# Kernel tuning notes

Measured on AMD Instinct MI355X. Metric: run time of the kernel, lower is better.

## Reference

```python
import jax, jax.numpy as jnp
import numpy as np

B, S, H, I, E, K = 2, 512, 512, 1024, 64, 4


def setup_inputs() -> dict:
    key = jax.random.key(0)
    ks = jax.random.split(key, 16)
    scale = jnp.float32(0.02)

    def w(k, shape):
        return jax.random.normal(k, shape, dtype=jnp.float32) * scale

    return {
        "x": jax.random.normal(ks[0], (B, S, H), dtype=jnp.float32),
        "router_w": w(ks[1], (E, H)),
        "router_b": w(ks[2], (E,)),
        "expert_biases": jnp.zeros((E,), dtype=jnp.float32),
        "sw1": w(ks[3], (I, H)), "sb1": w(ks[4], (I,)),
        "sw2": w(ks[5], (H, I)), "sb2": w(ks[6], (H,)),
        "sw3": w(ks[7], (I, H)), "sb3": w(ks[8], (I,)),
        "w1": w(ks[9], (E, I, H)), "b1": w(ks[10], (E, I)),
        "w2": w(ks[11], (E, H, I)), "b2": w(ks[12], (E, H)),
        "w3": w(ks[13], (E, I, H)), "b3": w(ks[14], (E, I)),
        "top_k": K,
    }


def _ffn(x, w1, b1, w2, b2, w3, b3):
    return (jax.nn.silu(x @ w1.T + b1) * (x @ w3.T + b3)) @ w2.T + b2


def reference(x, router_w, router_b, expert_biases,
              sw1, sb1, sw2, sb2, sw3, sb3,
              w1, b1, w2, b2, w3, b3, top_k):
    Bx, Sx, Hx = x.shape
    Ex = router_w.shape[0]

    # Router: logits [B,S,E]; top-k selection uses bias-adjusted logits,
    # but gates come from the ORIGINAL (unbiased) logits.
    logits = x @ router_w.T + router_b
    _, idx = jax.lax.top_k(logits + expert_biases, top_k)  # [B,S,K] int32
    orig = jnp.take_along_axis(logits, idx, axis=-1)       # [B,S,K]
    scores = jax.nn.sigmoid(orig)
    gates = scores / jnp.maximum(jnp.sum(scores, axis=-1, keepdims=True), 1e-12)

    # Shared expert(s): num_shared_experts == 1, divided by 1.
    shared = _ffn(x, sw1, sb1, sw2, sb2, sw3, sb3)

    # Combine gates into a dense per-token per-expert gate matrix [T,E].
    xf = x.reshape(-1, Hx)                 # [T,H]
    T = xf.shape[0]
    tok = jnp.arange(T)[:, None]
    gate_full = jnp.zeros((T, Ex), x.dtype).at[tok, idx.reshape(T, top_k)].add(
        gates.reshape(T, top_k))

    # Routed experts: each expert FFN over all tokens, gated combine.
    # (Mathematically identical to the original masked-dense loop: the mask
    #  zeroes both inputs and gates of unassigned tokens.)
    def body(acc, p):
        ew1, eb1, ew2, eb2, ew3, eb3, g = p
        y = _ffn(xf, ew1, eb1, ew2, eb2, ew3, eb3)  # [T,H]
        return acc + g[:, None] * y, None

    acc, _ = jax.lax.scan(body, jnp.zeros_like(xf),
                          (w1, b1, w2, b2, w3, b3, gate_full.T))

    return shared + acc.reshape(x.shape)
```

## Files before the change

kernel.cpp:

```cpp
#include <hip/hip_runtime.h>
#include <math.h>

#define T_    1024
#define H_    512
#define I_    1024
#define E_    64
#define K_    4
#define NPAIR (T_*K_)
#define NENT  (NPAIR + T_)

#define BM 64
#define BN 64
#define BKS 64
#define LDP 72
#define MAXWORK 160

typedef float  f32x4  __attribute__((ext_vector_type(4)));
typedef short  bf16x8 __attribute__((ext_vector_type(8)));

__device__ __forceinline__ ushort f2bf(float f) {
    uint u = __float_as_uint(f);
    u += 0x7fffu + ((u >> 16) & 1u);
    return (ushort)(u >> 16);
}

__global__ __launch_bounds__(64) void moe_router(
    const float* __restrict__ x, const float* __restrict__ rw,
    const float* __restrict__ rb, const float* __restrict__ eb,
    int* __restrict__ idx_out, float* __restrict__ gate_out)
{
    const int t = blockIdx.x;
    const int lane = threadIdx.x;
    __shared__ float xs[H_];
    __shared__ float lg[E_];
    __shared__ float bs[E_];
    for (int i = lane; i < H_; i += 64) xs[i] = x[(size_t)t*H_ + i];
    bs[lane] = eb[lane];
    __syncthreads();
    float acc = 0.f;
    const float* wrow = rw + (size_t)lane*H_;
    for (int k = 0; k < H_; k += 4) {
        float4 w4 = *reinterpret_cast<const float4*>(wrow + k);
        acc = fmaf(xs[k+0], w4.x, acc);
        acc = fmaf(xs[k+1], w4.y, acc);
        acc = fmaf(xs[k+2], w4.z, acc);
        acc = fmaf(xs[k+3], w4.w, acc);
    }
    lg[lane] = acc + rb[lane];
    __syncthreads();
    if (lane == 0) {
        unsigned long long used = 0ull;
        int sel[K_]; float orig[K_];
        for (int k = 0; k < K_; ++k) {
            float best = -INFINITY; int bi = 0;
            for (int e = 0; e < E_; ++e) {
                if (used & (1ull << e)) continue;
                float v = lg[e] + bs[e];
                if (v > best) { best = v; bi = e; }
            }
            used |= (1ull << bi);
            sel[k] = bi; orig[k] = lg[bi];
        }
        float s[K_]; float sum = 0.f;
        for (int k = 0; k < K_; ++k) { s[k] = 1.f/(1.f + __expf(-orig[k])); sum += s[k]; }
        sum = fmaxf(sum, 1e-12f);
        for (int k = 0; k < K_; ++k) {
            idx_out[t*K_ + k] = sel[k];
            gate_out[t*K_ + k] = s[k] / sum;
        }
    }
}

__global__ __launch_bounds__(256) void moe_build(
    const int* __restrict__ idx, const float* __restrict__ gates,
    int* __restrict__ cnts, int* __restrict__ offs,
    int* __restrict__ entry_token, float* __restrict__ entry_gate,
    int* __restrict__ pair_pos,
    int* __restrict__ blk_e, int* __restrict__ blk_ro, int* __restrict__ nwork)
{
    __shared__ int c[E_];
    __shared__ int run[E_];
    const int tid = threadIdx.x;
    if (tid < E_) c[tid] = 0;
    __syncthreads();
    for (int p = tid; p < NPAIR; p += 256) atomicAdd(&c[idx[p]], 1);
    __syncthreads();
    if (tid == 0) {
        int o = 0;
        for (int e = 0; e < E_; ++e) { run[e] = o; offs[e] = o; cnts[e] = c[e]; o += c[e]; }
        offs[E_] = NPAIR;
        cnts[E_] = T_;
        int nb = 0;
        for (int e = 0; e <= E_; ++e) {
            int n = (e < E_) ? c[e] : T_;
            for (int ro = 0; ro < n; ro += BM) { blk_e[nb] = e; blk_ro[nb] = ro; ++nb; }
        }
        nwork[0] = nb;
    }
    __syncthreads();
    for (int p = tid; p < NPAIR; p += 256) {
        int e = idx[p];
        int pos = atomicAdd(&run[e], 1);
        entry_token[pos] = p / K_;
        entry_gate[pos]  = gates[p];
        pair_pos[p]      = pos;
    }
    for (int t = tid; t < T_; t += 256) {
        entry_token[NPAIR + t] = t;
        entry_gate[NPAIR + t]  = 1.0f;
    }
}

__global__ __launch_bounds__(256) void moe_stage1(
    const float* __restrict__ x,
    const float* __restrict__ w1, const float* __restrict__ b1,
    const float* __restrict__ w3, const float* __restrict__ b3,
    const float* __restrict__ sw1, const float* __restrict__ sb1,
    const float* __restrict__ sw3, const float* __restrict__ sb3,
    const int* __restrict__ cnts, const int* __restrict__ offs,
    const int* __restrict__ entry_token,
    const int* __restrict__ blk_e, const int* __restrict__ blk_ro,
    const int* __restrict__ nwork,
    ushort* __restrict__ h1buf)
{
    const int w = blockIdx.x;
    if (w >= nwork[0]) return;
    const int e  = blk_e[w];
    const int ro = blk_ro[w];
    const int itile = blockIdx.y;
    const int n = cnts[e];
    const int off = offs[e];
    const int rows = min(BM, n - ro);
    const float* W1 = (e < E_) ? (w1 + (size_t)e*I_*H_) : sw1;
    const float* W3 = (e < E_) ? (w3 + (size_t)e*I_*H_) : sw3;
    const float* B1 = (e < E_) ? (b1 + (size_t)e*I_) : sb1;
    const float* B3 = (e < E_) ? (b3 + (size_t)e*I_) : sb3;

    __shared__ ushort Xs [BM][LDP];
    __shared__ ushort W1s[BN][LDP];
    __shared__ ushort W3s[BN][LDP];

    const int tid  = threadIdx.x;
    const int lane = tid & 63;
    const int wid  = tid >> 6;
    const int wm   = wid >> 1;
    const int wn   = wid & 1;
    const int l15  = lane & 15;
    const int lg   = lane >> 4;

    f32x4 acc1[2][2] = {};
    f32x4 acc3[2][2] = {};

    for (int kc = 0; kc < H_; kc += BKS) {
        __syncthreads();
        #pragma unroll
        for (int i = 0; i < 4; ++i) {
            int u = tid + i*256;
            int r = u >> 4, seg = u & 15;
            float4 v = make_float4(0.f,0.f,0.f,0.f);
            if (r < rows) {
                int tok = entry_token[off + ro + r];
                v = *reinterpret_cast<const float4*>(x + (size_t)tok*H_ + kc + seg*4);
            }
            *reinterpret_cast<ushort4*>(&Xs[r][seg*4]) =
                make_ushort4(f2bf(v.x), f2bf(v.y), f2bf(v.z), f2bf(v.w));
        }
        #pragma unroll
        for (int i = 0; i < 4; ++i) {
            int u = tid + i*256;
            int r = u >> 4, seg = u & 15;
            size_t go = (size_t)(itile*BN + r)*H_ + kc + seg*4;
            float4 v1 = *reinterpret_cast<const float4*>(W1 + go);
            float4 v3 = *reinterpret_cast<const float4*>(W3 + go);
            *reinterpret_cast<ushort4*>(&W1s[r][seg*4]) =
                make_ushort4(f2bf(v1.x), f2bf(v1.y), f2bf(v1.z), f2bf(v1.w));
            *reinterpret_cast<ushort4*>(&W3s[r][seg*4]) =
                make_ushort4(f2bf(v3.x), f2bf(v3.y), f2bf(v3.z), f2bf(v3.w));
        }
        __syncthreads();
        #pragma unroll
        for (int s = 0; s < 2; ++s) {
            bf16x8 a[2], bb1[2], bb3[2];
            #pragma unroll
            for (int f = 0; f < 2; ++f) {
                a[f]   = *reinterpret_cast<const bf16x8*>(&Xs [wm*32 + f*16 + l15][s*32 + lg*8]);
                bb1[f] = *reinterpret_cast<const bf16x8*>(&W1s[wn*32 + f*16 + l15][s*32 + lg*8]);
                bb3[f] = *reinterpret_cast<const bf16x8*>(&W3s[wn*32 + f*16 + l15][s*32 + lg*8]);
            }
            #pragma unroll
            for (int fm = 0; fm < 2; ++fm) {
                #pragma unroll
                for (int fn = 0; fn < 2; ++fn) {
                    acc1[fm][fn] = __builtin_amdgcn_mfma_f32_16x16x32_bf16(a[fm], bb1[fn], acc1[fm][fn], 0, 0, 0);
                    acc3[fm][fn] = __builtin_amdgcn_mfma_f32_16x16x32_bf16(a[fm], bb3[fn], acc3[fm][fn], 0, 0, 0);
                }
            }
        }
    }
    #pragma unroll
    for (int fm = 0; fm < 2; ++fm) {
        #pragma unroll
        for (int fn = 0; fn < 2; ++fn) {
            const int col = itile*BN + wn*32 + fn*16 + l15;
            const float bv1 = B1[col];
            const float bv3 = B3[col];
            #pragma unroll
            for (int j = 0; j < 4; ++j) {
                const int rl = wm*32 + fm*16 + lg*4 + j;
                if (rl < rows) {
                    float z1 = acc1[fm][fn][j] + bv1;
                    float z3 = acc3[fm][fn][j] + bv3;
                    float h = z1 / (1.f + __expf(-z1)) * z3;
                    h1buf[(size_t)(off+ro+rl)*I_ + col] = f2bf(h);
                }
            }
        }
    }
}

__global__ __launch_bounds__(256) void moe_stage2(
    const ushort* __restrict__ h1buf,
    const float* __restrict__ w2, const float* __restrict__ b2,
    const float* __restrict__ sw2, const float* __restrict__ sb2,
    const int* __restrict__ cnts, const int* __restrict__ offs,
    const float* __restrict__ entry_gate,
    const int* __restrict__ blk_e, const int* __restrict__ blk_ro,
    const int* __restrict__ nwork,
    float* __restrict__ ybuf)
{
    const int w = blockIdx.x;
    if (w >= nwork[0]) return;
    const int e  = blk_e[w];
    const int ro = blk_ro[w];
    const int htile = blockIdx.y;
    const int n = cnts[e];
    const int off = offs[e];
    const int rows = min(BM, n - ro);
    const float* W2 = (e < E_) ? (w2 + (size_t)e*H_*I_) : sw2;
    const float* B2 = (e < E_) ? (b2 + (size_t)e*H_) : sb2;

    __shared__ ushort Hs[BM][LDP];
    __shared__ ushort Ws[BN][LDP];

    const int tid  = threadIdx.x;
    const int lane = tid & 63;
    const int wid  = tid >> 6;
    const int wm   = wid >> 1;
    const int wn   = wid & 1;
    const int l15  = lane & 15;
    const int lg   = lane >> 4;

    f32x4 acc[2][2] = {};

    for (int kc = 0; kc < I_; kc += BKS) {
        __syncthreads();
        #pragma unroll
        for (int i = 0; i < 2; ++i) {
            int u = tid + i*256;
            int r = u >> 3, seg = u & 7;
            uint4 v = make_uint4(0u,0u,0u,0u);
            if (r < rows)
                v = *reinterpret_cast<const uint4*>(h1buf + (size_t)(off+ro+r)*I_ + kc + seg*8);
            *reinterpret_cast<uint4*>(&Hs[r][seg*8]) = v;
        }
        #pragma unroll
        for (int i = 0; i < 4; ++i) {
            int u = tid + i*256;
            int r = u >> 4, seg = u & 15;
            size_t go = (size_t)(htile*BN + r)*I_ + kc + seg*4;
            float4 v = *reinterpret_cast<const float4*>(W2 + go);
            *reinterpret_cast<ushort4*>(&Ws[r][seg*4]) =
                make_ushort4(f2bf(v.x), f2bf(v.y), f2bf(v.z), f2bf(v.w));
        }
        __syncthreads();
        #pragma unroll
        for (int s = 0; s < 2; ++s) {
            bf16x8 a[2], b[2];
            #pragma unroll
            for (int f = 0; f < 2; ++f) {
                a[f] = *reinterpret_cast<const bf16x8*>(&Hs[wm*32 + f*16 + l15][s*32 + lg*8]);
                b[f] = *reinterpret_cast<const bf16x8*>(&Ws[wn*32 + f*16 + l15][s*32 + lg*8]);
            }
            #pragma unroll
            for (int fm = 0; fm < 2; ++fm) {
                #pragma unroll
                for (int fn = 0; fn < 2; ++fn) {
                    acc[fm][fn] = __builtin_amdgcn_mfma_f32_16x16x32_bf16(a[fm], b[fn], acc[fm][fn], 0, 0, 0);
                }
            }
        }
    }
    #pragma unroll
    for (int fm = 0; fm < 2; ++fm) {
        #pragma unroll
        for (int fn = 0; fn < 2; ++fn) {
            const int col = htile*BN + wn*32 + fn*16 + l15;
            const float bv = B2[col];
            #pragma unroll
            for (int j = 0; j < 4; ++j) {
                const int rl = wm*32 + fm*16 + lg*4 + j;
                if (rl < rows) {
                    const float g = entry_gate[off + ro + rl];
                    ybuf[(size_t)(off+ro+rl)*H_ + col] = (acc[fm][fn][j] + bv) * g;
                }
            }
        }
    }
}

__global__ __launch_bounds__(128) void moe_combine(
    const float* __restrict__ ybuf, const int* __restrict__ pair_pos,
    float* __restrict__ out)
{
    const int t = blockIdx.x;
    const int lane = threadIdx.x;
    const int h = lane * 4;
    const int p0 = pair_pos[t*K_+0], p1 = pair_pos[t*K_+1];
    const int p2 = pair_pos[t*K_+2], p3 = pair_pos[t*K_+3];
    float4 a  = *reinterpret_cast<const float4*>(ybuf + (size_t)(NPAIR+t)*H_ + h);
    float4 v0 = *reinterpret_cast<const float4*>(ybuf + (size_t)p0*H_ + h);
    float4 v1 = *reinterpret_cast<const float4*>(ybuf + (size_t)p1*H_ + h);
    float4 v2 = *reinterpret_cast<const float4*>(ybuf + (size_t)p2*H_ + h);
    float4 v3 = *reinterpret_cast<const float4*>(ybuf + (size_t)p3*H_ + h);
    float4 r;
    r.x = a.x + v0.x + v1.x + v2.x + v3.x;
    r.y = a.y + v0.y + v1.y + v2.y + v3.y;
    r.z = a.z + v0.z + v1.z + v2.z + v3.z;
    r.w = a.w + v0.w + v1.w + v2.w + v3.w;
    *reinterpret_cast<float4*>(out + (size_t)t*H_ + h) = r;
}

extern "C" void kernel_launch(void* const* d_in, const int* in_sizes, int n_in,
                              void* d_out, int out_size, void* d_ws, size_t ws_size,
                              hipStream_t stream)
{
    const float* x   = (const float*)d_in[0];
    const float* rw  = (const float*)d_in[1];
    const float* rb  = (const float*)d_in[2];
    const float* eb  = (const float*)d_in[3];
    const float* sw1 = (const float*)d_in[4];
    const float* sb1 = (const float*)d_in[5];
    const float* sw2 = (const float*)d_in[6];
    const float* sb2 = (const float*)d_in[7];
    const float* sw3 = (const float*)d_in[8];
    const float* sb3 = (const float*)d_in[9];
    const float* w1  = (const float*)d_in[10];
    const float* b1  = (const float*)d_in[11];
    const float* w2  = (const float*)d_in[12];
    const float* b2  = (const float*)d_in[13];
    const float* w3  = (const float*)d_in[14];
    const float* b3  = (const float*)d_in[15];
    float* out = (float*)d_out;

    char* p = (char*)d_ws;
    auto take = [&](size_t bytes) { char* q = p; p += (bytes + 255) & ~(size_t)255; return q; };
    int*    idxb  = (int*)   take((size_t)NPAIR*4);
    float*  gateb = (float*) take((size_t)NPAIR*4);
    int*    cnts  = (int*)   take((E_+1)*4);
    int*    offs  = (int*)   take((E_+1)*4);
    int*    etok  = (int*)   take((size_t)NENT*4);
    float*  egate = (float*) take((size_t)NENT*4);
    int*    ppos  = (int*)   take((size_t)NPAIR*4);
    int*    blk_e = (int*)   take((size_t)MAXWORK*4);
    int*    blk_ro= (int*)   take((size_t)MAXWORK*4);
    int*    nwork = (int*)   take(4);
    ushort* h1buf = (ushort*)take((size_t)NENT*I_*2);
    float*  ybuf  = (float*) take((size_t)NENT*H_*4);

    moe_router <<<T_, 64, 0, stream>>>(x, rw, rb, eb, idxb, gateb);
    moe_build  <<<1, 256, 0, stream>>>(idxb, gateb, cnts, offs, etok, egate, ppos,
                                       blk_e, blk_ro, nwork);
    moe_stage1 <<<dim3(MAXWORK, I_/BN), 256, 0, stream>>>(x, w1, b1, w3, b3,
                                                          sw1, sb1, sw3, sb3,
                                                          cnts, offs, etok,
                                                          blk_e, blk_ro, nwork, h1buf);
    moe_stage2 <<<dim3(MAXWORK, H_/BN), 256, 0, stream>>>(h1buf, w2, b2, sw2, sb2,
                                                          cnts, offs, egate,
                                                          blk_e, blk_ro, nwork, ybuf);
    moe_combine<<<T_, 128, 0, stream>>>(ybuf, ppos, out);
}
```

Measured before the change: 221.8 us.

## Drop LDS staging in the MoE GEMMs and feed MFMA from registers with prefetch

Both expert GEMM stages stop staging tiles through shared memory. Each wave now loads its own 16-column slice of weights straight from global memory into registers, double-buffered one step ahead and converted with packed bf16 instructions. Activation fragments are gathered directly from global memory or L2 for 128-row tiles. A new pre-pass converts x to bf16 once, so stage 1 gathers half-width rows, and the larger row tile means each expert's weights are re-read fewer times. The cost is redundant activation reads across the four waves, more register pressure from the 8-row-fragment accumulators, and reads of padding rows beyond each expert's count.

New measurement: 359.1 us. 1.62x slower.

```diff
diff --git a/kernel.cpp b/kernel.cpp
--- a/kernel.cpp
+++ b/kernel.cpp
@@ -9,11 +9,12 @@
 #define NPAIR (T_*K_)
 #define NENT  (NPAIR + T_)
 
-#define BM 64
+#define BM 128
 #define BN 64
-#define BKS 64
-#define LDP 72
+#define BKS 32
 #define MAXWORK 160
+#define NT1 (H_/BKS)
+#define NT2 (I_/BKS)
 
 typedef float  f32x4  __attribute__((ext_vector_type(4)));
 typedef short  bf16x8 __attribute__((ext_vector_type(8)));
@@ -22,6 +23,23 @@
     uint u = __float_as_uint(f);
     u += 0x7fffu + ((u >> 16) & 1u);
     return (ushort)(u >> 16);
+}
+__device__ __forceinline__ bf16x8 cvt8pk(f32x4 a, f32x4 b) {
+    union { uint u[4]; bf16x8 v; } r;
+    asm("v_cvt_pk_bf16_f32 %0, %1, %2" : "=v"(r.u[0]) : "v"(a[0]), "v"(a[1]));
+    asm("v_cvt_pk_bf16_f32 %0, %1, %2" : "=v"(r.u[1]) : "v"(a[2]), "v"(a[3]));
+    asm("v_cvt_pk_bf16_f32 %0, %1, %2" : "=v"(r.u[2]) : "v"(b[0]), "v"(b[1]));
+    asm("v_cvt_pk_bf16_f32 %0, %1, %2" : "=v"(r.u[3]) : "v"(b[2]), "v"(b[3]));
+    return r.v;
+}
+
+__global__ __launch_bounds__(256) void x_cvt(const float* __restrict__ x,
+                                             ushort* __restrict__ xb)
+{
+    const int i = blockIdx.x*256 + threadIdx.x;
+    float4 v = reinterpret_cast<const float4*>(x)[i];
+    reinterpret_cast<ushort4*>(xb)[i] =
+        make_ushort4(f2bf(v.x), f2bf(v.y), f2bf(v.z), f2bf(v.w));
 }
 
 __global__ __launch_bounds__(64) void moe_router(
@@ -111,8 +129,8 @@
     }
 }
 
-__global__ __launch_bounds__(256) void moe_stage1(
-    const float* __restrict__ x,
+__global__ __launch_bounds__(256, 2) void moe_stage1(
+    const ushort* __restrict__ xbf,
     const float* __restrict__ w1, const float* __restrict__ b1,
     const float* __restrict__ w3, const float* __restrict__ b3,
     const float* __restrict__ sw1, const float* __restrict__ sb1,
@@ -136,89 +154,72 @@
     const float* B1 = (e < E_) ? (b1 + (size_t)e*I_) : sb1;
     const float* B3 = (e < E_) ? (b3 + (size_t)e*I_) : sb3;
 
-    __shared__ ushort Xs [BM][LDP];
-    __shared__ ushort W1s[BN][LDP];
-    __shared__ ushort W3s[BN][LDP];
-
     const int tid  = threadIdx.x;
     const int lane = tid & 63;
     const int wid  = tid >> 6;
-    const int wm   = wid >> 1;
-    const int wn   = wid & 1;
     const int l15  = lane & 15;
     const int lg   = lane >> 4;
 
-    f32x4 acc1[2][2] = {};
-    f32x4 acc3[2][2] = {};
-
-    for (int kc = 0; kc < H_; kc += BKS) {
-        __syncthreads();
-        #pragma unroll
-        for (int i = 0; i < 4; ++i) {
-            int u = tid + i*256;
-            int r = u >> 4, seg = u & 15;
-            float4 v = make_float4(0.f,0.f,0.f,0.f);
-            if (r < rows) {
-                int tok = entry_token[off + ro + r];
-                v = *reinterpret_cast<const float4*>(x + (size_t)tok*H_ + kc + seg*4);
+    const ushort* ab[8];
+    #pragma unroll
+    for (int m = 0; m < 8; ++m) {
+        const int tok = entry_token[off + ro + m*16 + l15];
+        ab[m] = xbf + (size_t)tok*H_ + lg*8;
+    }
+    const int ncol = itile*BN + wid*16 + l15;
+    const float* b1p = W1 + (size_t)ncol*H_ + lg*8;
+    const float* b3p = W3 + (size_t)ncol*H_ + lg*8;
+
+    f32x4 acc1[8] = {};
+    f32x4 acc3[8] = {};
+
+    f32x4 s0[4], s1[4];
+
+    #define LW1(S, kc) do {                                      \
+        S[0] = *reinterpret_cast<const f32x4*>(b1p + (kc));      \
+        S[1] = *reinterpret_cast<const f32x4*>(b1p + (kc) + 4);  \
+        S[2] = *reinterpret_cast<const f32x4*>(b3p + (kc));      \
+        S[3] = *reinterpret_cast<const f32x4*>(b3p + (kc) + 4);  \
+    } while (0)
+
+    LW1(s0, 0);
+    #pragma unroll
+    for (int t = 0; t < NT1; ++t) {
+        const int kc = t*BKS;
+        bf16x8 a[8];
+        #pragma unroll
+        for (int m = 0; m < 8; ++m)
+            a[m] = *reinterpret_cast<const bf16x8*>(ab[m] + kc);
+        if (t + 1 < NT1) { if (t & 1) LW1(s0, kc + BKS); else LW1(s1, kc + BKS); }
+        bf16x8 f1, f3;
+        if (t & 1) { f1 = cvt8pk(s1[0], s1[1]); f3 = cvt8pk(s1[2], s1[3]); }
+        else       { f1 = cvt8pk(s0[0], s0[1]); f3 = cvt8pk(s0[2], s0[3]); }
+        #pragma unroll
+        for (int m = 0; m < 8; ++m) {
+            acc1[m] = __builtin_amdgcn_mfma_f32_16x16x32_bf16(a[m], f1, acc1[m], 0, 0, 0);
+            acc3[m] = __builtin_amdgcn_mfma_f32_16x16x32_bf16(a[m], f3, acc3[m], 0, 0, 0);
+        }
+    }
+    #undef LW1
+
+    const float bv1 = B1[ncol];
+    const float bv3 = B3[ncol];
+    #pragma unroll
+    for (int m = 0; m < 8; ++m) {
+        #pragma unroll
+        for (int j = 0; j < 4; ++j) {
+            const int rl = m*16 + lg*4 + j;
+            if (rl < rows) {
+                float z1 = acc1[m][j] + bv1;
+                float z3 = acc3[m][j] + bv3;
+                float h = z1 / (1.f + __expf(-z1)) * z3;
+                h1buf[(size_t)(off+ro+rl)*I_ + ncol] = f2bf(h);
             }
-            *reinterpret_cast<ushort4*>(&Xs[r][seg*4]) =
-                make_ushort4(f2bf(v.x), f2bf(v.y), f2bf(v.z), f2bf(v.w));
-        }
-        #pragma unroll
-        for (int i = 0; i < 4; ++i) {
-            int u = tid + i*256;
-            int r = u >> 4, seg = u & 15;
-            size_t go = (size_t)(itile*BN + r)*H_ + kc + seg*4;
-            float4 v1 = *reinterpret_cast<const float4*>(W1 + go);
-            float4 v3 = *reinterpret_cast<const float4*>(W3 + go);
-            *reinterpret_cast<ushort4*>(&W1s[r][seg*4]) =
-                make_ushort4(f2bf(v1.x), f2bf(v1.y), f2bf(v1.z), f2bf(v1.w));
-            *reinterpret_cast<ushort4*>(&W3s[r][seg*4]) =
-                make_ushort4(f2bf(v3.x), f2bf(v3.y), f2bf(v3.z), f2bf(v3.w));
-        }
-        __syncthreads();
-        #pragma unroll
-        for (int s = 0; s < 2; ++s) {
-            bf16x8 a[2], bb1[2], bb3[2];
-            #pragma unroll
-            for (int f = 0; f < 2; ++f) {
-                a[f]   = *reinterpret_cast<const bf16x8*>(&Xs [wm*32 + f*16 + l15][s*32 + lg*8]);
-                bb1[f] = *reinterpret_cast<const bf16x8*>(&W1s[wn*32 + f*16 + l15][s*32 + lg*8]);
-                bb3[f] = *reinterpret_cast<const bf16x8*>(&W3s[wn*32 + f*16 + l15][s*32 + lg*8]);
-            }
-            #pragma unroll
-            for (int fm = 0; fm < 2; ++fm) {
-                #pragma unroll
-                for (int fn = 0; fn < 2; ++fn) {
-                    acc1[fm][fn] = __builtin_amdgcn_mfma_f32_16x16x32_bf16(a[fm], bb1[fn], acc1[fm][fn], 0, 0, 0);
-                    acc3[fm][fn] = __builtin_amdgcn_mfma_f32_16x16x32_bf16(a[fm], bb3[fn], acc3[fm][fn], 0, 0, 0);
-                }
-            }
-        }
-    }
-    #pragma unroll
-    for (int fm = 0; fm < 2; ++fm) {
-        #pragma unroll
-        for (int fn = 0; fn < 2; ++fn) {
-            const int col = itile*BN + wn*32 + fn*16 + l15;
-            const float bv1 = B1[col];
-            const float bv3 = B3[col];
-            #pragma unroll
-            for (int j = 0; j < 4; ++j) {
-                const int rl = wm*32 + fm*16 + lg*4 + j;
-                if (rl < rows) {
-                    float z1 = acc1[fm][fn][j] + bv1;
-                    float z3 = acc3[fm][fn][j] + bv3;
-                    float h = z1 / (1.f + __expf(-z1)) * z3;
-                    h1buf[(size_t)(off+ro+rl)*I_ + col] = f2bf(h);
-                }
-            }
-        }
-    }
-}
-
-__global__ __launch_bounds__(256) void moe_stage2(
+        }
+    }
+}
+
+__global__ __launch_bounds__(256, 2) void moe_stage2(
     const ushort* __restrict__ h1buf,
     const float* __restrict__ w2, const float* __restrict__ b2,
     const float* __restrict__ sw2, const float* __restrict__ sb2,
@@ -239,70 +240,55 @@
     const float* W2 = (e < E_) ? (w2 + (size_t)e*H_*I_) : sw2;
     const float* B2 = (e < E_) ? (b2 + (size_t)e*H_) : sb2;
 
-    __shared__ ushort Hs[BM][LDP];
-    __shared__ ushort Ws[BN][LDP];
-
     const int tid  = threadIdx.x;
     const int lane = tid & 63;
     const int wid  = tid >> 6;
-    const int wm   = wid >> 1;
-    const int wn   = wid & 1;
     const int l15  = lane & 15;
     const int lg   = lane >> 4;
 
-    f32x4 acc[2][2] = {};
-
-    for (int kc = 0; kc < I_; kc += BKS) {
-        __syncthreads();
-        #pragma unroll
-        for (int i = 0; i < 2; ++i) {
-            int u = tid + i*256;
-            int r = u >> 3, seg = u & 7;
-            uint4 v = make_uint4(0u,0u,0u,0u);
-            if (r < rows)
-                v = *reinterpret_cast<const uint4*>(h1buf + (size_t)(off+ro+r)*I_ + kc + seg*8);
-            *reinterpret_cast<uint4*>(&Hs[r][seg*8]) = v;
-        }
-        #pragma unroll
-        for (int i = 0; i < 4; ++i) {
-            int u = tid + i*256;
-            int r = u >> 4, seg = u & 15;
-            size_t go = (size_t)(htile*BN + r)*I_ + kc + seg*4;
-            float4 v = *reinterpret_cast<const float4*>(W2 + go);
-            *reinterpret_cast<ushort4*>(&Ws[r][seg*4]) =
-                make_ushort4(f2bf(v.x), f2bf(v.y), f2bf(v.z), f2bf(v.w));
-        }
-        __syncthreads();
-        #pragma unroll
-        for (int s = 0; s < 2; ++s) {
-            bf16x8 a[2], b[2];
-            #pragma unroll
-            for (int f = 0; f < 2; ++f) {
-                a[f] = *reinterpret_cast<const bf16x8*>(&Hs[wm*32 + f*16 + l15][s*32 + lg*8]);
-                b[f] = *reinterpret_cast<const bf16x8*>(&Ws[wn*32 + f*16 + l15][s*32 + lg*8]);
-            }
-            #pragma unroll
-            for (int fm = 0; fm < 2; ++fm) {
-                #pragma unroll
-                for (int fn = 0; fn < 2; ++fn) {
-                    acc[fm][fn] = __builtin_amdgcn_mfma_f32_16x16x32_bf16(a[fm], b[fn], acc[fm][fn], 0, 0, 0);
-                }
-            }
-        }
-    }
-    #pragma unroll
-    for (int fm = 0; fm < 2; ++fm) {
-        #pragma unroll
-        for (int fn = 0; fn < 2; ++fn) {
-            const int col = htile*BN + wn*32 + fn*16 + l15;
-            const float bv = B2[col];
-            #pragma unroll
-            for (int j = 0; j < 4; ++j) {
-                const int rl = wm*32 + fm*16 + lg*4 + j;
-                if (rl < rows) {
-                    const float g = entry_gate[off + ro + rl];
-                    ybuf[(size_t)(off+ro+rl)*H_ + col] = (acc[fm][fn][j] + bv) * g;
-                }
+    const ushort* ab[8];
+    #pragma unroll
+    for (int m = 0; m < 8; ++m)
+        ab[m] = h1buf + (size_t)(off + ro + m*16 + l15)*I_ + lg*8;
+    const int ncol = htile*BN + wid*16 + l15;
+    const float* bp = W2 + (size_t)ncol*I_ + lg*8;
+
+    f32x4 acc[8] = {};
+
+    f32x4 s0[2], s1[2];
+
+    #define LW2(S, kc) do {                                     \
+        S[0] = *reinterpret_cast<const f32x4*>(bp + (kc));      \
+        S[1] = *reinterpret_cast<const f32x4*>(bp + (kc) + 4);  \
+    } while (0)
+
+    LW2(s0, 0);
+    #pragma unroll
+    for (int t = 0; t < NT2; ++t) {
+        const int kc = t*BKS;
+        bf16x8 a[8];
+        #pragma unroll
+        for (int m = 0; m < 8; ++m)
+            a[m] = *reinterpret_cast<const bf16x8*>(ab[m] + kc);
+        if (t + 1 < NT2) { if (t & 1) LW2(s0, kc + BKS); else LW2(s1, kc + BKS); }
+        bf16x8 f;
+        if (t & 1) f = cvt8pk(s1[0], s1[1]);
+        else       f = cvt8pk(s0[0], s0[1]);
+        #pragma unroll
+        for (int m = 0; m < 8; ++m)
+            acc[m] = __builtin_amdgcn_mfma_f32_16x16x32_bf16(a[m], f, acc[m], 0, 0, 0);
+    }
+    #undef LW2
+
+    const float bv = B2[ncol];
+    #pragma unroll
+    for (int m = 0; m < 8; ++m) {
+        #pragma unroll
+        for (int j = 0; j < 4; ++j) {
+            const int rl = m*16 + lg*4 + j;
+            if (rl < rows) {
+                const float g = entry_gate[off + ro + rl];
+                ybuf[(size_t)(off+ro+rl)*H_ + ncol] = (acc[m][j] + bv) * g;
             }
         }
     }
@@ -364,13 +350,15 @@
     int*    blk_e = (int*)   take((size_t)MAXWORK*4);
     int*    blk_ro= (int*)   take((size_t)MAXWORK*4);
     int*    nwork = (int*)   take(4);
+    ushort* xbf   = (ushort*)take((size_t)T_*H_*2);
     ushort* h1buf = (ushort*)take((size_t)NENT*I_*2);
     float*  ybuf  = (float*) take((size_t)NENT*H_*4);
 
+    x_cvt      <<<(T_*H_)/(256*4), 256, 0, stream>>>(x, xbf);
     moe_router <<<T_, 64, 0, stream>>>(x, rw, rb, eb, idxb, gateb);
     moe_build  <<<1, 256, 0, stream>>>(idxb, gateb, cnts, offs, etok, egate, ppos,
                                        blk_e, blk_ro, nwork);
-    moe_stage1 <<<dim3(MAXWORK, I_/BN), 256, 0, stream>>>(x, w1, b1, w3, b3,
+    moe_stage1 <<<dim3(MAXWORK, I_/BN), 256, 0, stream>>>(xbf, w1, b1, w3, b3,
                                                           sw1, sb1, sw3, sb3,
                                                           cnts, offs, etok,
                                                           blk_e, blk_ro, nwork, h1buf);
```

## Retile expert GEMMs to 128x32 with 512 threads and register-prefetch pipelining

Applied to the files above, without the earlier changes.

Both expert GEMM stages switch from 64x64 tiles with 256 threads to 128-row by 32-column tiles with 512 threads. Each stage now prefetches the next K-slice into registers while the current slice is consumed from LDS. A new pre-pass converts x to bf16 once, so stage1 gathers bf16 rows instead of converting fp32 on every tile. The grid axes are swapped so that blocks sharing an expert's token tile launch next to each other. Loads no longer check the row bound and may read neighbouring experts' rows, which are discarded; the cost is an extra kernel launch and a larger workspace.

Result: slower. 247.9 us (+11.8%).

```diff
diff --git a/kernel.cpp b/kernel.cpp
--- a/kernel.cpp
+++ b/kernel.cpp
@@ -9,11 +9,13 @@
 #define NPAIR (T_*K_)
 #define NENT  (NPAIR + T_)
 
-#define BM 64
-#define BN 64
+#define BM 128
+#define BN 32
 #define BKS 64
 #define LDP 72
 #define MAXWORK 160
+#define NT1 (H_/BKS)
+#define NT2 (I_/BKS)
 
 typedef float  f32x4  __attribute__((ext_vector_type(4)));
 typedef short  bf16x8 __attribute__((ext_vector_type(8)));
@@ -22,6 +24,18 @@
     uint u = __float_as_uint(f);
     u += 0x7fffu + ((u >> 16) & 1u);
     return (ushort)(u >> 16);
+}
+__device__ __forceinline__ ushort4 cvt4(float4 v) {
+    return make_ushort4(f2bf(v.x), f2bf(v.y), f2bf(v.z), f2bf(v.w));
+}
+
+__global__ __launch_bounds__(256) void x_cvt(const float* __restrict__ x,
+                                             ushort* __restrict__ xb)
+{
+    const int i = blockIdx.x*256 + threadIdx.x;
+    float4 v = reinterpret_cast<const float4*>(x)[i];
+    reinterpret_cast<ushort4*>(xb)[i] =
+        make_ushort4(f2bf(v.x), f2bf(v.y), f2bf(v.z), f2bf(v.w));
 }
 
 __global__ __launch_bounds__(64) void moe_router(
@@ -111,8 +125,8 @@
     }
 }
 
-__global__ __launch_bounds__(256) void moe_stage1(
-    const float* __restrict__ x,
+__global__ __launch_bounds__(512, 6) void moe_stage1(
+    const ushort* __restrict__ xbf,
     const float* __restrict__ w1, const float* __restrict__ b1,
     const float* __restrict__ w3, const float* __restrict__ b3,
     const float* __restrict__ sw1, const float* __restrict__ sb1,
@@ -123,11 +137,11 @@
     const int* __restrict__ nwork,
     ushort* __restrict__ h1buf)
 {
-    const int w = blockIdx.x;
+    const int w = blockIdx.y;
     if (w >= nwork[0]) return;
     const int e  = blk_e[w];
     const int ro = blk_ro[w];
-    const int itile = blockIdx.y;
+    const int itile = blockIdx.x;
     const int n = cnts[e];
     const int off = offs[e];
     const int rows = min(BM, n - ro);
@@ -148,77 +162,80 @@
     const int l15  = lane & 15;
     const int lg   = lane >> 4;
 
-    f32x4 acc1[2][2] = {};
-    f32x4 acc3[2][2] = {};
-
-    for (int kc = 0; kc < H_; kc += BKS) {
+    const int xr = tid >> 3;
+    const int xc = tid & 7;
+    const int wr = tid >> 4;
+    const int wc = tid & 15;
+
+    const ushort* xp[2];
+    #pragma unroll
+    for (int i = 0; i < 2; ++i)
+        xp[i] = xbf + (size_t)entry_token[off + ro + xr + i*64]*H_ + xc*8;
+    const float* w1p = W1 + (size_t)(itile*BN + wr)*H_ + wc*4;
+    const float* w3p = W3 + (size_t)(itile*BN + wr)*H_ + wc*4;
+
+    f32x4 acc1[2] = {};
+    f32x4 acc3[2] = {};
+
+    uint4  hx[2];
+    float4 v1, v3;
+
+    auto issue = [&](int kc) {
+        #pragma unroll
+        for (int i = 0; i < 2; ++i)
+            hx[i] = *reinterpret_cast<const uint4*>(xp[i] + kc);
+        v1 = *reinterpret_cast<const float4*>(w1p + kc);
+        v3 = *reinterpret_cast<const float4*>(w3p + kc);
+    };
+    auto stwrite = [&]() {
+        #pragma unroll
+        for (int i = 0; i < 2; ++i)
+            *reinterpret_cast<uint4*>(&Xs[xr + i*64][xc*8]) = hx[i];
+        *reinterpret_cast<ushort4*>(&W1s[wr][wc*4]) = cvt4(v1);
+        *reinterpret_cast<ushort4*>(&W3s[wr][wc*4]) = cvt4(v3);
+    };
+
+    issue(0);
+    for (int t = 0; t < NT1; ++t) {
         __syncthreads();
-        #pragma unroll
-        for (int i = 0; i < 4; ++i) {
-            int u = tid + i*256;
-            int r = u >> 4, seg = u & 15;
-            float4 v = make_float4(0.f,0.f,0.f,0.f);
-            if (r < rows) {
-                int tok = entry_token[off + ro + r];
-                v = *reinterpret_cast<const float4*>(x + (size_t)tok*H_ + kc + seg*4);
-            }
-            *reinterpret_cast<ushort4*>(&Xs[r][seg*4]) =
-                make_ushort4(f2bf(v.x), f2bf(v.y), f2bf(v.z), f2bf(v.w));
-        }
-        #pragma unroll
-        for (int i = 0; i < 4; ++i) {
-            int u = tid + i*256;
-            int r = u >> 4, seg = u & 15;
-            size_t go = (size_t)(itile*BN + r)*H_ + kc + seg*4;
-            float4 v1 = *reinterpret_cast<const float4*>(W1 + go);
-            float4 v3 = *reinterpret_cast<const float4*>(W3 + go);
-            *reinterpret_cast<ushort4*>(&W1s[r][seg*4]) =
-                make_ushort4(f2bf(v1.x), f2bf(v1.y), f2bf(v1.z), f2bf(v1.w));
-            *reinterpret_cast<ushort4*>(&W3s[r][seg*4]) =
-                make_ushort4(f2bf(v3.x), f2bf(v3.y), f2bf(v3.z), f2bf(v3.w));
-        }
+        stwrite();
+        if (t + 1 < NT1) issue((t + 1)*BKS);
         __syncthreads();
         #pragma unroll
         for (int s = 0; s < 2; ++s) {
-            bf16x8 a[2], bb1[2], bb3[2];
+            bf16x8 a[2], bb1, bb3;
+            #pragma unroll
+            for (int f = 0; f < 2; ++f)
+                a[f] = *reinterpret_cast<const bf16x8*>(&Xs[wm*32 + f*16 + l15][s*32 + lg*8]);
+            bb1 = *reinterpret_cast<const bf16x8*>(&W1s[wn*16 + l15][s*32 + lg*8]);
+            bb3 = *reinterpret_cast<const bf16x8*>(&W3s[wn*16 + l15][s*32 + lg*8]);
             #pragma unroll
             for (int f = 0; f < 2; ++f) {
-                a[f]   = *reinterpret_cast<const bf16x8*>(&Xs [wm*32 + f*16 + l15][s*32 + lg*8]);
-                bb1[f] = *reinterpret_cast<const bf16x8*>(&W1s[wn*32 + f*16 + l15][s*32 + lg*8]);
-                bb3[f] = *reinterpret_cast<const bf16x8*>(&W3s[wn*32 + f*16 + l15][s*32 + lg*8]);
+                acc1[f] = __builtin_amdgcn_mfma_f32_16x16x32_bf16(a[f], bb1, acc1[f], 0, 0, 0);
+                acc3[f] = __builtin_amdgcn_mfma_f32_16x16x32_bf16(a[f], bb3, acc3[f], 0, 0, 0);
             }
-            #pragma unroll
-            for (int fm = 0; fm < 2; ++fm) {
-                #pragma unroll
-                for (int fn = 0; fn < 2; ++fn) {
-                    acc1[fm][fn] = __builtin_amdgcn_mfma_f32_16x16x32_bf16(a[fm], bb1[fn], acc1[fm][fn], 0, 0, 0);
-                    acc3[fm][fn] = __builtin_amdgcn_mfma_f32_16x16x32_bf16(a[fm], bb3[fn], acc3[fm][fn], 0, 0, 0);
-                }
+        }
+    }
+
+    const int col = itile*BN + wn*16 + l15;
+    const float bv1 = B1[col];
+    const float bv3 = B3[col];
+    #pragma unroll
+    for (int f = 0; f < 2; ++f) {
+        #pragma unroll
+        for (int j = 0; j < 4; ++j) {
+            const int rl = wm*32 + f*16 + lg*4 + j;
+            if (rl < rows) {
+                float z1 = acc1[f][j] + bv1;
+                float z3 = acc3[f][j] + bv3;
+                float h = z1 / (1.f + __expf(-z1)) * z3;
+                h1buf[(size_t)(off+ro+rl)*I_ + col] = f2bf(h);
             }
         }
     }
-    #pragma unroll
-    for (int fm = 0; fm < 2; ++fm) {
-        #pragma unroll
-        for (int fn = 0; fn < 2; ++fn) {
-            const int col = itile*BN + wn*32 + fn*16 + l15;
-            const float bv1 = B1[col];
-            const float bv3 = B3[col];
-            #pragma unroll
-            for (int j = 0; j < 4; ++j) {
-                const int rl = wm*32 + fm*16 + lg*4 + j;
-                if (rl < rows) {
-                    float z1 = acc1[fm][fn][j] + bv1;
-                    float z3 = acc3[fm][fn][j] + bv3;
-                    float h = z1 / (1.f + __expf(-z1)) * z3;
-                    h1buf[(size_t)(off+ro+rl)*I_ + col] = f2bf(h);
-                }
-            }
-        }
-    }
-}
-
-__global__ __launch_bounds__(256) void moe_stage2(
+}
+
+__global__ __launch_bounds__(512, 6) void moe_stage2(
     const ushort* __restrict__ h1buf,
     const float* __restrict__ w2, const float* __restrict__ b2,
     const float* __restrict__ sw2, const float* __restrict__ sb2,
@@ -228,11 +245,11 @@
     const int* __restrict__ nwork,
     float* __restrict__ ybuf)
 {
-    const int w = blockIdx.x;
+    const int w = blockIdx.y;
     if (w >= nwork[0]) return;
     const int e  = blk_e[w];
     const int ro = blk_ro[w];
-    const int htile = blockIdx.y;
+    const int htile = blockIdx.x;
     const int n = cnts[e];
     const int off = offs[e];
     const int rows = min(BM, n - ro);
@@ -250,59 +267,64 @@
     const int l15  = lane & 15;
     const int lg   = lane >> 4;
 
-    f32x4 acc[2][2] = {};
-
-    for (int kc = 0; kc < I_; kc += BKS) {
+    const int hr = tid >> 3;
+    const int hc = tid & 7;
+    const int wr = tid >> 4;
+    const int wc = tid & 15;
+
+    const ushort* hp[2];
+    #pragma unroll
+    for (int i = 0; i < 2; ++i)
+        hp[i] = h1buf + (size_t)(off + ro + hr + i*64)*I_ + hc*8;
+    const float* wp = W2 + (size_t)(htile*BN + wr)*I_ + wc*4;
+
+    f32x4 acc[2] = {};
+
+    uint4  hv[2];
+    float4 wv;
+
+    auto issue = [&](int kc) {
+        #pragma unroll
+        for (int i = 0; i < 2; ++i)
+            hv[i] = *reinterpret_cast<const uint4*>(hp[i] + kc);
+        wv = *reinterpret_cast<const float4*>(wp + kc);
+    };
+    auto stwrite = [&]() {
+        #pragma unroll
+        for (int i = 0; i < 2; ++i)
+            *reinterpret_cast<uint4*>(&Hs[hr + i*64][hc*8]) = hv[i];
+        *reinterpret_cast<ushort4*>(&Ws[wr][wc*4]) = cvt4(wv);
+    };
+
+    issue(0);
+    for (int t = 0; t < NT2; ++t) {
         __syncthreads();
-        #pragma unroll
-        for (int i = 0; i < 2; ++i) {
-            int u = tid + i*256;
-            int r = u >> 3, seg = u & 7;
-            uint4 v = make_uint4(0u,0u,0u,0u);
-            if (r < rows)
-                v = *reinterpret_cast<const uint4*>(h1buf + (size_t)(off+ro+r)*I_ + kc + seg*8);
-            *reinterpret_cast<uint4*>(&Hs[r][seg*8]) = v;
-        }
-        #pragma unroll
-        for (int i = 0; i < 4; ++i) {
-            int u = tid + i*256;
-            int r = u >> 4, seg = u & 15;
-            size_t go = (size_t)(htile*BN + r)*I_ + kc + seg*4;
-            float4 v = *reinterpret_cast<const float4*>(W2 + go);
-            *reinterpret_cast<ushort4*>(&Ws[r][seg*4]) =
-                make_ushort4(f2bf(v.x), f2bf(v.y), f2bf(v.z), f2bf(v.w));
-        }
+        stwrite();
+        if (t + 1 < NT2) issue((t + 1)*BKS);
         __syncthreads();
         #pragma unroll
         for (int s = 0; s < 2; ++s) {
-            bf16x8 a[2], b[2];
+            bf16x8 a[2], bb;
             #pragma unroll
-            for (int f = 0; f < 2; ++f) {
+            for (int f = 0; f < 2; ++f)
                 a[f] = *reinterpret_cast<const bf16x8*>(&Hs[wm*32 + f*16 + l15][s*32 + lg*8]);
-                b[f] = *reinterpret_cast<const bf16x8*>(&Ws[wn*32 + f*16 + l15][s*32 + lg*8]);
-            }
+            bb = *reinterpret_cast<const bf16x8*>(&Ws[wn*16 + l15][s*32 + lg*8]);
             #pragma unroll
-            for (int fm = 0; fm < 2; ++fm) {
-                #pragma unroll
-                for (int fn = 0; fn < 2; ++fn) {
-                    acc[fm][fn] = __builtin_amdgcn_mfma_f32_16x16x32_bf16(a[fm], b[fn], acc[fm][fn], 0, 0, 0);
-                }
-            }
-        }
-    }
+            for (int f = 0; f < 2; ++f)
+                acc[f] = __builtin_amdgcn_mfma_f32_16x16x32_bf16(a[f], bb, acc[f], 0, 0, 0);
+        }
+    }
+
+    const int col = htile*BN + wn*16 + l15;
+    const float bv = B2[col];
     #pragma unroll
-    for (int fm = 0; fm < 2; ++fm) {
-        #pragma unroll
-        for (int fn = 0; fn < 2; ++fn) {
-            const int col = htile*BN + wn*32 + fn*16 + l15;
-            const float bv = B2[col];
-            #pragma unroll
-            for (int j = 0; j < 4; ++j) {
-                const int rl = wm*32 + fm*16 + lg*4 + j;
-                if (rl < rows) {
-                    const float g = entry_gate[off + ro + rl];
-                    ybuf[(size_t)(off+ro+rl)*H_ + col] = (acc[fm][fn][j] + bv) * g;
-                }
+    for (int f = 0; f < 2; ++f) {
+        #pragma unroll
+        for (int j = 0; j < 4; ++j) {
+            const int rl = wm*32 + f*16 + lg*4 + j;
+            if (rl < rows) {
+                const float g = entry_gate[off + ro + rl];
+                ybuf[(size_t)(off+ro+rl)*H_ + col] = (acc[f][j] + bv) * g;
             }
         }
     }
@@ -364,17 +386,19 @@
     int*    blk_e = (int*)   take((size_t)MAXWORK*4);
     int*    blk_ro= (int*)   take((size_t)MAXWORK*4);
     int*    nwork = (int*)   take(4);
+    ushort* xbf   = (ushort*)take((size_t)T_*H_*2);
     ushort* h1buf = (ushort*)take((size_t)NENT*I_*2);
     float*  ybuf  = (float*) take((size_t)NENT*H_*4);
 
+    x_cvt      <<<(T_*H_)/(256*4), 256, 0, stream>>>(x, xbf);
     moe_router <<<T_, 64, 0, stream>>>(x, rw, rb, eb, idxb, gateb);
     moe_build  <<<1, 256, 0, stream>>>(idxb, gateb, cnts, offs, etok, egate, ppos,
                                        blk_e, blk_ro, nwork);
-    moe_stage1 <<<dim3(MAXWORK, I_/BN), 256, 0, stream>>>(x, w1, b1, w3, b3,
+    moe_stage1 <<<dim3(I_/BN, MAXWORK), 512, 0, stream>>>(xbf, w1, b1, w3, b3,
                                                           sw1, sb1, sw3, sb3,
                                                           cnts, offs, etok,
                                                           blk_e, blk_ro, nwork, h1buf);
-    moe_stage2 <<<dim3(MAXWORK, H_/BN), 256, 0, stream>>>(h1buf, w2, b2, sw2, sb2,
+    moe_stage2 <<<dim3(H_/BN, MAXWORK), 512, 0, stream>>>(h1buf, w2, b2, sw2, sb2,
                                                           cnts, offs, egate,
                                                           blk_e, blk_ro, nwork, ybuf);
     moe_combine<<<T_, 128, 0, stream>>>(ybuf, ppos, out);
```

## Pre-pack gathered bf16 activations and stage full-K weight slabs in swizzled LDS

Applied to the files above, without the earlier changes.

Adds a pass that gathers each routed token row once and stores it as bf16. Both expert GEMM stages now use 128-row by 32-column tiles with 512 threads. Each block loads its whole K-extent weight slab into LDS once, using an XOR swizzle to avoid bank conflicts, and then streams MFMAs reading the A operand straight from global memory, with no per-chunk barriers. The aim is to cut the repeated gather and fp32 conversion of x, and the many synchronisations per K chunk. The cost is 64KB of LDS per block, which limits occupancy, plus uncached global A loads that can read past the valid rows (those results are masked out).

Result: slower. 231.4 us (+4.3%).

```diff
diff --git a/kernel.cpp b/kernel.cpp
--- a/kernel.cpp
+++ b/kernel.cpp
@@ -9,10 +9,8 @@
 #define NPAIR (T_*K_)
 #define NENT  (NPAIR + T_)
 
-#define BM 64
-#define BN 64
-#define BKS 64
-#define LDP 72
+#define BM 128
+#define BN 32
 #define MAXWORK 160
 
 typedef float  f32x4  __attribute__((ext_vector_type(4)));
@@ -22,6 +20,9 @@
     uint u = __float_as_uint(f);
     u += 0x7fffu + ((u >> 16) & 1u);
     return (ushort)(u >> 16);
+}
+__device__ __forceinline__ ushort4 cvt4(f32x4 v) {
+    return make_ushort4(f2bf(v[0]), f2bf(v[1]), f2bf(v[2]), f2bf(v[3]));
 }
 
 __global__ __launch_bounds__(64) void moe_router(
@@ -111,23 +112,34 @@
     }
 }
 
-__global__ __launch_bounds__(256) void moe_stage1(
-    const float* __restrict__ x,
+__global__ __launch_bounds__(128) void moe_xpack(
+    const float* __restrict__ x, const int* __restrict__ entry_token,
+    ushort* __restrict__ xg)
+{
+    const int row = blockIdx.x;
+    const int tok = entry_token[row];
+    const int c = threadIdx.x * 4;
+    float4 v = *reinterpret_cast<const float4*>(x + (size_t)tok*H_ + c);
+    *reinterpret_cast<ushort4*>(xg + (size_t)row*H_ + c) =
+        make_ushort4(f2bf(v.x), f2bf(v.y), f2bf(v.z), f2bf(v.w));
+}
+
+__global__ __launch_bounds__(512, 4) void moe_stage1(
+    const ushort* __restrict__ xg,
     const float* __restrict__ w1, const float* __restrict__ b1,
     const float* __restrict__ w3, const float* __restrict__ b3,
     const float* __restrict__ sw1, const float* __restrict__ sb1,
     const float* __restrict__ sw3, const float* __restrict__ sb3,
     const int* __restrict__ cnts, const int* __restrict__ offs,
-    const int* __restrict__ entry_token,
     const int* __restrict__ blk_e, const int* __restrict__ blk_ro,
     const int* __restrict__ nwork,
     ushort* __restrict__ h1buf)
 {
-    const int w = blockIdx.x;
+    const int w = blockIdx.y;
     if (w >= nwork[0]) return;
     const int e  = blk_e[w];
     const int ro = blk_ro[w];
-    const int itile = blockIdx.y;
+    const int itile = blockIdx.x;
     const int n = cnts[e];
     const int off = offs[e];
     const int rows = min(BM, n - ro);
@@ -136,89 +148,70 @@
     const float* B1 = (e < E_) ? (b1 + (size_t)e*I_) : sb1;
     const float* B3 = (e < E_) ? (b3 + (size_t)e*I_) : sb3;
 
-    __shared__ ushort Xs [BM][LDP];
-    __shared__ ushort W1s[BN][LDP];
-    __shared__ ushort W3s[BN][LDP];
+    __shared__ __align__(16) ushort W1L[BN*H_];
+    __shared__ __align__(16) ushort W3L[BN*H_];
 
     const int tid  = threadIdx.x;
     const int lane = tid & 63;
     const int wid  = tid >> 6;
-    const int wm   = wid >> 1;
-    const int wn   = wid & 1;
     const int l15  = lane & 15;
     const int lg   = lane >> 4;
 
-    f32x4 acc1[2][2] = {};
-    f32x4 acc3[2][2] = {};
-
-    for (int kc = 0; kc < H_; kc += BKS) {
-        __syncthreads();
-        #pragma unroll
-        for (int i = 0; i < 4; ++i) {
-            int u = tid + i*256;
-            int r = u >> 4, seg = u & 15;
-            float4 v = make_float4(0.f,0.f,0.f,0.f);
-            if (r < rows) {
-                int tok = entry_token[off + ro + r];
-                v = *reinterpret_cast<const float4*>(x + (size_t)tok*H_ + kc + seg*4);
+    {
+        const f32x4* s1 = reinterpret_cast<const f32x4*>(W1 + (size_t)(itile*BN)*H_);
+        const f32x4* s3 = reinterpret_cast<const f32x4*>(W3 + (size_t)(itile*BN)*H_);
+        #pragma unroll
+        for (int i = 0; i < 8; ++i) {
+            const int f4 = i*512 + tid;
+            f32x4 v1 = s1[f4];
+            f32x4 v3 = s3[f4];
+            const int row = f4 >> 7;
+            const int c8  = f4 & 127;
+            const int byte = row*1024 + (((c8 >> 1) ^ (row & 7)) << 4) + (c8 & 1)*8;
+            *reinterpret_cast<ushort4*>((char*)W1L + byte) = cvt4(v1);
+            *reinterpret_cast<ushort4*>((char*)W3L + byte) = cvt4(v3);
+        }
+    }
+    __syncthreads();
+
+    const ushort* ap = xg + (size_t)(off + ro + wid*16 + l15)*H_ + lg*8;
+
+    f32x4 acc1[2] = {};
+    f32x4 acc3[2] = {};
+
+    #pragma unroll
+    for (int t = 0; t < 16; ++t) {
+        bf16x8 a = *reinterpret_cast<const bf16x8*>(ap + t*32);
+        #pragma unroll
+        for (int fn = 0; fn < 2; ++fn) {
+            const int rw = fn*16 + l15;
+            const int byte = rw*1024 + ((((t << 2) | lg) ^ (rw & 7)) << 4);
+            bf16x8 bb1 = *reinterpret_cast<const bf16x8*>((const char*)W1L + byte);
+            bf16x8 bb3 = *reinterpret_cast<const bf16x8*>((const char*)W3L + byte);
+            acc1[fn] = __builtin_amdgcn_mfma_f32_16x16x32_bf16(a, bb1, acc1[fn], 0, 0, 0);
+            acc3[fn] = __builtin_amdgcn_mfma_f32_16x16x32_bf16(a, bb3, acc3[fn], 0, 0, 0);
+        }
+    }
+
+    #pragma unroll
+    for (int fn = 0; fn < 2; ++fn) {
+        const int col = itile*BN + fn*16 + l15;
+        const float bv1 = B1[col];
+        const float bv3 = B3[col];
+        #pragma unroll
+        for (int j = 0; j < 4; ++j) {
+            const int rl = wid*16 + lg*4 + j;
+            if (rl < rows) {
+                float z1 = acc1[fn][j] + bv1;
+                float z3 = acc3[fn][j] + bv3;
+                float h = z1 / (1.f + __expf(-z1)) * z3;
+                h1buf[(size_t)(off+ro+rl)*I_ + col] = f2bf(h);
             }
-            *reinterpret_cast<ushort4*>(&Xs[r][seg*4]) =
-                make_ushort4(f2bf(v.x), f2bf(v.y), f2bf(v.z), f2bf(v.w));
-        }
-        #pragma unroll
-        for (int i = 0; i < 4; ++i) {
-            int u = tid + i*256;
-            int r = u >> 4, seg = u & 15;
-            size_t go = (size_t)(itile*BN + r)*H_ + kc + seg*4;
-            float4 v1 = *reinterpret_cast<const float4*>(W1 + go);
-            float4 v3 = *reinterpret_cast<const float4*>(W3 + go);
-            *reinterpret_cast<ushort4*>(&W1s[r][seg*4]) =
-                make_ushort4(f2bf(v1.x), f2bf(v1.y), f2bf(v1.z), f2bf(v1.w));
-            *reinterpret_cast<ushort4*>(&W3s[r][seg*4]) =
-                make_ushort4(f2bf(v3.x), f2bf(v3.y), f2bf(v3.z), f2bf(v3.w));
-        }
-        __syncthreads();
-        #pragma unroll
-        for (int s = 0; s < 2; ++s) {
-            bf16x8 a[2], bb1[2], bb3[2];
-            #pragma unroll
-            for (int f = 0; f < 2; ++f) {
-                a[f]   = *reinterpret_cast<const bf16x8*>(&Xs [wm*32 + f*16 + l15][s*32 + lg*8]);
-                bb1[f] = *reinterpret_cast<const bf16x8*>(&W1s[wn*32 + f*16 + l15][s*32 + lg*8]);
-                bb3[f] = *reinterpret_cast<const bf16x8*>(&W3s[wn*32 + f*16 + l15][s*32 + lg*8]);
-            }
-            #pragma unroll
-            for (int fm = 0; fm < 2; ++fm) {
-                #pragma unroll
-                for (int fn = 0; fn < 2; ++fn) {
-                    acc1[fm][fn] = __builtin_amdgcn_mfma_f32_16x16x32_bf16(a[fm], bb1[fn], acc1[fm][fn], 0, 0, 0);
-                    acc3[fm][fn] = __builtin_amdgcn_mfma_f32_16x16x32_bf16(a[fm], bb3[fn], acc3[fm][fn], 0, 0, 0);
-                }
-            }
-        }
-    }
-    #pragma unroll
-    for (int fm = 0; fm < 2; ++fm) {
-        #pragma unroll
-        for (int fn = 0; fn < 2; ++fn) {
-            const int col = itile*BN + wn*32 + fn*16 + l15;
-            const float bv1 = B1[col];
-            const float bv3 = B3[col];
-            #pragma unroll
-            for (int j = 0; j < 4; ++j) {
-                const int rl = wm*32 + fm*16 + lg*4 + j;
-                if (rl < rows) {
-                    float z1 = acc1[fm][fn][j] + bv1;
-                    float z3 = acc3[fm][fn][j] + bv3;
-                    float h = z1 / (1.f + __expf(-z1)) * z3;
-                    h1buf[(size_t)(off+ro+rl)*I_ + col] = f2bf(h);
-                }
-            }
-        }
-    }
-}
-
-__global__ __launch_bounds__(256) void moe_stage2(
+        }
+    }
+}
+
+__global__ __launch_bounds__(512, 4) void moe_stage2(
     const ushort* __restrict__ h1buf,
     const float* __restrict__ w2, const float* __restrict__ b2,
     const float* __restrict__ sw2, const float* __restrict__ sb2,
@@ -228,81 +221,65 @@
     const int* __restrict__ nwork,
     float* __restrict__ ybuf)
 {
-    const int w = blockIdx.x;
+    const int w = blockIdx.y;
     if (w >= nwork[0]) return;
     const int e  = blk_e[w];
     const int ro = blk_ro[w];
-    const int htile = blockIdx.y;
+    const int htile = blockIdx.x;
     const int n = cnts[e];
     const int off = offs[e];
     const int rows = min(BM, n - ro);
     const float* W2 = (e < E_) ? (w2 + (size_t)e*H_*I_) : sw2;
     const float* B2 = (e < E_) ? (b2 + (size_t)e*H_) : sb2;
 
-    __shared__ ushort Hs[BM][LDP];
-    __shared__ ushort Ws[BN][LDP];
+    __shared__ __align__(16) ushort W2L[BN*I_];
 
     const int tid  = threadIdx.x;
     const int lane = tid & 63;
     const int wid  = tid >> 6;
-    const int wm   = wid >> 1;
-    const int wn   = wid & 1;
     const int l15  = lane & 15;
     const int lg   = lane >> 4;
 
-    f32x4 acc[2][2] = {};
-
-    for (int kc = 0; kc < I_; kc += BKS) {
-        __syncthreads();
-        #pragma unroll
-        for (int i = 0; i < 2; ++i) {
-            int u = tid + i*256;
-            int r = u >> 3, seg = u & 7;
-            uint4 v = make_uint4(0u,0u,0u,0u);
-            if (r < rows)
-                v = *reinterpret_cast<const uint4*>(h1buf + (size_t)(off+ro+r)*I_ + kc + seg*8);
-            *reinterpret_cast<uint4*>(&Hs[r][seg*8]) = v;
-        }
-        #pragma unroll
-        for (int i = 0; i < 4; ++i) {
-            int u = tid + i*256;
-            int r = u >> 4, seg = u & 15;
-            size_t go = (size_t)(htile*BN + r)*I_ + kc + seg*4;
-            float4 v = *reinterpret_cast<const float4*>(W2 + go);
-            *reinterpret_cast<ushort4*>(&Ws[r][seg*4]) =
-                make_ushort4(f2bf(v.x), f2bf(v.y), f2bf(v.z), f2bf(v.w));
-        }
-        __syncthreads();
-        #pragma unroll
-        for (int s = 0; s < 2; ++s) {
-            bf16x8 a[2], b[2];
-            #pragma unroll
-            for (int f = 0; f < 2; ++f) {
-                a[f] = *reinterpret_cast<const bf16x8*>(&Hs[wm*32 + f*16 + l15][s*32 + lg*8]);
-                b[f] = *reinterpret_cast<const bf16x8*>(&Ws[wn*32 + f*16 + l15][s*32 + lg*8]);
-            }
-            #pragma unroll
-            for (int fm = 0; fm < 2; ++fm) {
-                #pragma unroll
-                for (int fn = 0; fn < 2; ++fn) {
-                    acc[fm][fn] = __builtin_amdgcn_mfma_f32_16x16x32_bf16(a[fm], b[fn], acc[fm][fn], 0, 0, 0);
-                }
-            }
-        }
-    }
+    {
+        const f32x4* s2 = reinterpret_cast<const f32x4*>(W2 + (size_t)(htile*BN)*I_);
+        #pragma unroll
+        for (int i = 0; i < 16; ++i) {
+            const int f4 = i*512 + tid;
+            f32x4 v = s2[f4];
+            const int row = f4 >> 8;
+            const int c8  = f4 & 255;
+            const int byte = row*2048 + (((c8 >> 1) ^ (row & 7)) << 4) + (c8 & 1)*8;
+            *reinterpret_cast<ushort4*>((char*)W2L + byte) = cvt4(v);
+        }
+    }
+    __syncthreads();
+
+    const ushort* ap = h1buf + (size_t)(off + ro + wid*16 + l15)*I_ + lg*8;
+
+    f32x4 acc[2] = {};
+
     #pragma unroll
-    for (int fm = 0; fm < 2; ++fm) {
+    for (int t = 0; t < 32; ++t) {
+        bf16x8 a = *reinterpret_cast<const bf16x8*>(ap + t*32);
         #pragma unroll
         for (int fn = 0; fn < 2; ++fn) {
-            const int col = htile*BN + wn*32 + fn*16 + l15;
-            const float bv = B2[col];
-            #pragma unroll
-            for (int j = 0; j < 4; ++j) {
-                const int rl = wm*32 + fm*16 + lg*4 + j;
-                if (rl < rows) {
-                    const float g = entry_gate[off + ro + rl];
-                    ybuf[(size_t)(off+ro+rl)*H_ + col] = (acc[fm][fn][j] + bv) * g;
-                }
+            const int rw = fn*16 + l15;
+            const int byte = rw*2048 + ((((t << 2) | lg) ^ (rw & 7)) << 4);
+            bf16x8 bb = *reinterpret_cast<const bf16x8*>((const char*)W2L + byte);
+            acc[fn] = __builtin_amdgcn_mfma_f32_16x16x32_bf16(a, bb, acc[fn], 0, 0, 0);
+        }
+    }
+
+    #pragma unroll
+    for (int fn = 0; fn < 2; ++fn) {
+        const int col = htile*BN + fn*16 + l15;
+        const float bv = B2[col];
+        #pragma unroll
+        for (int j = 0; j < 4; ++j) {
+            const int rl = wid*16 + lg*4 + j;
+            if (rl < rows) {
+                const float g = entry_gate[off + ro + rl];
+                ybuf[(size_t)(off+ro+rl)*H_ + col] = (acc[fn][j] + bv) * g;
             }
         }
     }
@@ -364,17 +341,19 @@
     int*    blk_e = (int*)   take((size_t)MAXWORK*4);
     int*    blk_ro= (int*)   take((size_t)MAXWORK*4);
     int*    nwork = (int*)   take(4);
+    ushort* xg    = (ushort*)take((size_t)NENT*H_*2);
     ushort* h1buf = (ushort*)take((size_t)NENT*I_*2);
     float*  ybuf  = (float*) take((size_t)NENT*H_*4);
 
     moe_router <<<T_, 64, 0, stream>>>(x, rw, rb, eb, idxb, gateb);
     moe_build  <<<1, 256, 0, stream>>>(idxb, gateb, cnts, offs, etok, egate, ppos,
                                        blk_e, blk_ro, nwork);
-    moe_stage1 <<<dim3(MAXWORK, I_/BN), 256, 0, stream>>>(x, w1, b1, w3, b3,
+    moe_xpack  <<<NENT, 128, 0, stream>>>(x, etok, xg);
+    moe_stage1 <<<dim3(I_/BN, MAXWORK), 512, 0, stream>>>(xg, w1, b1, w3, b3,
                                                           sw1, sb1, sw3, sb3,
-                                                          cnts, offs, etok,
+                                                          cnts, offs,
                                                           blk_e, blk_ro, nwork, h1buf);
-    moe_stage2 <<<dim3(MAXWORK, H_/BN), 256, 0, stream>>>(h1buf, w2, b2, sw2, sb2,
+    moe_stage2 <<<dim3(H_/BN, MAXWORK), 512, 0, stream>>>(h1buf, w2, b2, sw2, sb2,
                                                           cnts, offs, egate,
                                                           blk_e, blk_ro, nwork, ybuf);
     moe_combine<<<T_, 128, 0, stream>>>(ybuf, ppos, out);
```
